# Kernel tuning notes

Measured on AMD Instinct MI355X. Metric: run time of the kernel, lower is better.

Reference implementation:

```python
import jax, jax.numpy as jnp
import numpy as np

NH = 1024
VS = 50257
CUT0 = 1675          # round(VS/30)
CUT1 = 3 * CUT0      # 5025
N_CLUSTERS = 2
HEAD_SIZE = CUT0 + N_CLUSTERS          # 1677
D0, D1 = NH // 4, NH // 16             # 256, 64
SZ0, SZ1 = CUT1 - CUT0, VS - CUT1      # 3350, 45232


def setup_inputs() -> dict:
    key = jax.random.key(0)
    ks = jax.random.split(key, 8)
    s = 0.02
    return {
        "x": jax.random.normal(ks[0], (8, 512, NH), dtype=jnp.float32),
        "y": jax.random.randint(ks[1], (8, 512), 0, VS, dtype=jnp.int64),
        "head_w": jax.random.normal(ks[2], (HEAD_SIZE, NH), dtype=jnp.float32) * s,
        "head_b": jnp.zeros((HEAD_SIZE,), dtype=jnp.float32),
        "proj0": jax.random.normal(ks[3], (D0, NH), dtype=jnp.float32) * s,
        "w0": jax.random.normal(ks[4], (SZ0, D0), dtype=jnp.float32) * s,
        "proj1": jax.random.normal(ks[5], (D1, NH), dtype=jnp.float32) * s,
        "w1": jax.random.normal(ks[6], (SZ1, D1), dtype=jnp.float32) * s,
    }


def reference(x, y, head_w, head_b, proj0, w0, proj1, w1):
    # Flatten as in the torch forward: x -> [N, nh], y -> [N]
    xf = x.reshape(-1, x.shape[-1])            # [N, NH]
    yf = y.reshape(-1)                         # [N]

    # Head: shortlist tokens + 2 cluster logits
    head_logits = jnp.einsum('nh,vh->nv', xf, head_w) + head_b   # [N, 1677]
    head_lp = jax.nn.log_softmax(head_logits, axis=-1)

    # Default: target in head shortlist
    in_head = yf < CUT0
    idx_head = jnp.where(in_head, yf, 0)
    out = jnp.take_along_axis(head_lp, idx_head[:, None], axis=1)[:, 0]

    # Tail clusters: dense per-cluster small GEMMs + log-softmax, masked select
    for i, (low, high, proj, w) in enumerate(
            [(CUT0, CUT1, proj0, w0), (CUT1, VS, proj1, w1)]):
        size = high - low
        h = jnp.einsum('nh,dh->nd', xf, proj)          # [N, d_i]
        lp = jax.nn.log_softmax(jnp.einsum('nd,vd->nv', h, w), axis=-1)  # [N, size]
        rel = jnp.clip(yf - low, 0, size - 1)
        cl = head_lp[:, CUT0 + i] + jnp.take_along_axis(lp, rel[:, None], axis=1)[:, 0]
        mask = (yf >= low) & (yf < high)
        out = jnp.where(mask, cl, out)

    loss = -jnp.mean(out)
    return out, loss
```

## Files before the change

kernel.cpp:

```cpp
#include <hip/hip_runtime.h>
#include <stdint.h>

#define NROWS 4096
#define NHID 1024
#define CC0 1675
#define CC1 5025
#define HEADSZ 1677
#define PD0 256
#define PD1 64
#define TSZ0 3350
#define TSZ1 45232
#define HPN (HEADSZ + PD0 + PD1)
#define TPC1 6
#define L2E 1.4426950408889634f
#define LN2 0.6931471805599453f

#define NB_HD 896
#define NB_PJ 192
#define NB_CW 512
#define NB_MID (NB_HD + NB_PJ + NB_CW)

#define NB_C1 1888
#define NB_C0 864
#define NB_TG 1024
#define NB_TAIL (NB_C1 + NB_C0 + NB_TG)

typedef __attribute__((ext_vector_type(8))) __bf16 bf16x8;
typedef __attribute__((ext_vector_type(4))) float f32x4;

__device__ __forceinline__ unsigned short f2bf(float f) {
  union { float f; uint32_t u; } v; v.f = f;
  return (unsigned short)((v.u + 0x7FFFu + ((v.u >> 16) & 1u)) >> 16);
}
__device__ __forceinline__ float bfl(uint32_t u) {
  union { uint32_t u; float f; } v; v.u = u << 16; return v.f;
}
__device__ __forceinline__ float bfh(uint32_t u) {
  union { uint32_t u; float f; } v; v.u = u & 0xFFFF0000u; return v.f;
}
__device__ __forceinline__ float bf1(unsigned short u) {
  union { uint32_t u; float f; } v; v.u = ((uint32_t)u) << 16; return v.f;
}
#define EXP2(x) __builtin_amdgcn_exp2f(x)

#define CV1 1048576
#define CV2 1477888
#define CV3 1543424
#define CV4 1559808
#define CV5 1774208
#define CV6 2497920
#define CVW0 (CV5 - CV4)
#define CVW  (CV6 - CV4)

__global__ void conv_part(const float* __restrict__ x, const float* __restrict__ hw,
                          const float* __restrict__ p0, const float* __restrict__ p1,
                          unsigned short* __restrict__ dst,
                          const int* __restrict__ y,
                          int* __restrict__ idx0, int* __restrict__ pos0,
                          int* __restrict__ idx1, int* __restrict__ pos1,
                          int* __restrict__ n01,
                          float* __restrict__ hs3, float* __restrict__ outp) {
  if (blockIdx.x >= 1025) {
    int z = blockIdx.x - 1025;
    for (int i = z * 256 + (int)threadIdx.x; i < 3 * NROWS; i += 7 * 256)
      hs3[i] = 0.f;
    if (z == 0 && threadIdx.x == 0) outp[NROWS] = 0.f;
    return;
  }
  if (blockIdx.x == 1024) {
    __shared__ int sc0[256], sc1[256], nsh[2];
    int t = threadIdx.x;
    int yl[16];
    int c0 = 0, c1 = 0;
#pragma unroll
    for (int k = 0; k < 16; ++k) {
      int yv = y[t * 16 + k];
      yl[k] = yv;
      c0 += (yv >= CC0 && yv < CC1);
      c1 += (yv >= CC1);
    }
    sc0[t] = c0; sc1[t] = c1;
    __syncthreads();
    if (t == 0) {
      int a0 = 0, a1 = 0;
      for (int i = 0; i < 256; ++i) {
        int v0 = sc0[i]; sc0[i] = a0; a0 += v0;
        int v1 = sc1[i]; sc1[i] = a1; a1 += v1;
      }
      n01[0] = a0; n01[1] = a1; nsh[0] = a0; nsh[1] = a1;
    }
    __syncthreads();
    int p0c = sc0[t], p1c = sc1[t];
#pragma unroll
    for (int k = 0; k < 16; ++k) {
      int n = t * 16 + k, yv = yl[k];
      if (yv >= CC0 && yv < CC1) { idx0[p0c] = n; pos0[n] = p0c; ++p0c; }
      else if (yv >= CC1)        { idx1[p1c] = n; pos1[n] = p1c; ++p1c; }
    }
    for (int j = nsh[0] + t; j < NROWS; j += 256) idx0[j] = 0;
    for (int j = nsh[1] + t; j < NROWS; j += 256) idx1[j] = 0;
    return;
  }
  const int stride = 1024 * 256;
  for (int i = blockIdx.x * 256 + threadIdx.x; i < CV4; i += stride) {
    const float* src; int off; float sc;
    if (i < CV1)      { src = x;  off = i;       sc = 1.f; }
    else if (i < CV2) { src = hw; off = i - CV1; sc = L2E; }
    else if (i < CV3) { src = p0; off = i - CV2; sc = 1.f; }
    else              { src = p1; off = i - CV3; sc = 1.f; }
    float4 v = reinterpret_cast<const float4*>(src)[off];
    ushort4 o;
    o.x = f2bf(v.x * sc); o.y = f2bf(v.y * sc);
    o.z = f2bf(v.z * sc); o.w = f2bf(v.w * sc);
    reinterpret_cast<ushort4*>(dst)[i] = o;
  }
}

#define GLOAD(g, l) __builtin_amdgcn_global_load_lds( \
    (const __attribute__((address_space(1))) uint32_t*)(const void*)(g), \
    (__attribute__((address_space(3))) uint32_t*)(void*)(l), 16, 0, 0)

#define SWZB(L) ((L) ^ ((((L) >> 7) & 7) << 4))

__device__ __forceinline__
void gemm_core(const unsigned short* __restrict__ A, int lda,
               const unsigned short* __restrict__ B, int ldb,
               int N, int K, int tile0, int tile1, int brow,
               const float* __restrict__ bias,
               float* __restrict__ sum_out,
               unsigned short* __restrict__ Cout, int ldc, int coutStart,
               unsigned short* AsB, unsigned short* BsB,
               const int* __restrict__ gidx) {
  const int tid = threadIdx.x;
  const int lane = tid & 63;
  const int wid = tid >> 6;
  const int wrow = (wid >> 1) * 64;
  const int wcol = (wid & 1) * 64;
  const int lr = lane & 15, lg = lane >> 4;
  const int nsteps = (tile1 - tile0) * (K >> 5);
  const int rowBase = brow + wrow;

  int arowc[2];
#pragma unroll
  for (int c = 0; c < 2; ++c) {
    int g = wid * 128 + c * 64 + lane;
    int S = SWZB(g * 16);
    int row = S >> 6;
    arowc[c] = gidx ? gidx[brow + row] : brow + row;
  }

  float sacc[4][4];
#pragma unroll
  for (int m = 0; m < 4; ++m)
#pragma unroll
    for (int r = 0; r < 4; ++r) sacc[m][r] = 0.f;

  auto stage = [&](int b, int tt, int kk) {
#pragma unroll
    for (int c = 0; c < 2; ++c) {
      int g = wid * 128 + c * 64 + lane;
      int L = g * 16;
      int S = SWZB(L);
      int row = S >> 6, ko = (S >> 4) & 3;
      GLOAD(A + (size_t)arowc[c] * lda + kk + ko * 8, (char*)AsB + b * 8192 + L);
      int bsrc = tt * 128 + row; bsrc = bsrc < N ? bsrc : N - 1;
      GLOAD(B + (size_t)bsrc * ldb + kk + ko * 8, (char*)BsB + b * 8192 + L);
    }
  };

  f32x4 acc[4][4];
#pragma unroll
  for (int m = 0; m < 4; ++m)
#pragma unroll
    for (int n = 0; n < 4; ++n) acc[m][n] = (f32x4){0.f, 0.f, 0.f, 0.f};

  int tp = tile0, kp = 0;
  auto adv = [&](int& t, int& k) { k += 32; if (k == K) { k = 0; ++t; } };
  stage(0, tp, kp); adv(tp, kp);
  if (nsteps > 1) { stage(1, tp, kp); adv(tp, kp); }

  int tile = tile0, k0 = 0;
  for (int s = 0; s < nsteps; ++s) {
    if (s + 1 < nsteps) asm volatile("s_waitcnt vmcnt(4)" ::: "memory");
    else                asm volatile("s_waitcnt vmcnt(0)" ::: "memory");
    __builtin_amdgcn_s_barrier();
    if (s + 2 < nsteps) { stage((s + 2) % 3, tp, kp); adv(tp, kp); }

    const int cur = s % 3;
    int k0n = k0 + 32, tn = tile;
    if (k0n == K) { k0n = 0; tn = tile + 1; }

    bf16x8 af[4], bfv[4];
#pragma unroll
    for (int m = 0; m < 4; ++m)
      af[m] = *(const bf16x8*)((const char*)AsB + cur * 8192 +
                               SWZB((wrow + m * 16 + lr) * 64 + lg * 16));
#pragma unroll
    for (int n = 0; n < 4; ++n)
      bfv[n] = *(const bf16x8*)((const char*)BsB + cur * 8192 +
                                SWZB((wcol + n * 16 + lr) * 64 + lg * 16));
#pragma unroll
    for (int m = 0; m < 4; ++m)
#pragma unroll
      for (int n = 0; n < 4; ++n)
        acc[m][n] = __builtin_amdgcn_mfma_f32_16x16x32_bf16(af[m], bfv[n], acc[m][n], 0, 0, 0);

    if (tn != tile) {
      const int cb = tile * 128 + wcol;
#pragma unroll
      for (int m = 0; m < 4; ++m)
#pragma unroll
        for (int n = 0; n < 4; ++n) {
#pragma unroll
          for (int r = 0; r < 4; ++r) {
            int col = cb + n * 16 + lr;
            if (col < N) {
              float v = acc[m][n][r];
              if (Cout && col >= coutStart) {
                int row = rowBase + m * 16 + lg * 4 + r;
                Cout[(size_t)row * ldc + (col - coutStart)] = f2bf(v);
              } else {
                if (bias) v = fmaf(bias[col], L2E, v);
                sacc[m][r] += EXP2(v);
              }
            }
          }
          acc[m][n] = (f32x4){0.f, 0.f, 0.f, 0.f};
        }
    }
    tile = tn; k0 = k0n;
  }

#pragma unroll
  for (int m = 0; m < 4; ++m)
#pragma unroll
    for (int r = 0; r < 4; ++r) {
      float s = sacc[m][r];
      s += __shfl_xor(s, 1); s += __shfl_xor(s, 2);
      s += __shfl_xor(s, 4); s += __shfl_xor(s, 8);
      if (lr == 0) atomicAdd(&sum_out[rowBase + m * 16 + lg * 4 + r], s);
    }
}

__device__ __forceinline__
void gemm_core4(const unsigned short* __restrict__ A, int lda,
                const unsigned short* __restrict__ B, int ldb,
                int N, int K, int tile0, int brow,
                const float* __restrict__ bias,
                float* __restrict__ sum_out,
                unsigned short* __restrict__ Cout, int ldc,
                char* AsB, char* BsB) {
  const int tid = threadIdx.x;
  const int lane = tid & 63;
  const int wid = tid >> 6;
  const int wrow = (wid >> 1) * 32;
  const int wcol = (wid & 1) * 64;
  const int lr = lane & 15, lg = lane >> 4;
  const int nsteps = K >> 5;
  const int rowBase = brow + wrow;

  const int aL = tid * 16;
  const int aS = SWZB(aL);
  const int arow = aS >> 6, ako = ((aS >> 4) & 3) * 8;
  int bcol[2], bko[2];
#pragma unroll
  for (int c = 0; c < 2; ++c) {
    int L = (c * 256 + tid) * 16;
    int S = SWZB(L);
    int col = S >> 6;
    int bsrc = tile0 * 128 + col;
    bcol[c] = bsrc < N ? bsrc : N - 1;
    bko[c] = ((S >> 4) & 3) * 8;
  }

  auto stage = [&](int b, int kk) {
    GLOAD(A + (size_t)(brow + arow) * lda + kk + ako, AsB + b * 4096 + aL);
#pragma unroll
    for (int c = 0; c < 2; ++c)
      GLOAD(B + (size_t)bcol[c] * ldb + kk + bko[c],
            BsB + b * 8192 + (c * 256 + tid) * 16);
  };

  f32x4 acc[2][4];
#pragma unroll
  for (int m = 0; m < 2; ++m)
#pragma unroll
    for (int n = 0; n < 4; ++n) acc[m][n] = (f32x4){0.f, 0.f, 0.f, 0.f};

  stage(0, 0);
  stage(1, 32);

  for (int s = 0; s < nsteps; ++s) {
    if (s + 1 < nsteps) asm volatile("s_waitcnt vmcnt(3)" ::: "memory");
    else                asm volatile("s_waitcnt vmcnt(0)" ::: "memory");
    __builtin_amdgcn_s_barrier();
    if (s + 2 < nsteps) stage((s + 2) % 3, (s + 2) * 32);

    const int cur = s % 3;
    bf16x8 af[2], bfv[4];
#pragma unroll
    for (int m = 0; m < 2; ++m)
      af[m] = *(const bf16x8*)(AsB + cur * 4096 +
                               SWZB((wrow + m * 16 + lr) * 64 + lg * 16));
#pragma unroll
    for (int n = 0; n < 4; ++n)
      bfv[n] = *(const bf16x8*)(BsB + cur * 8192 +
                                SWZB((wcol + n * 16 + lr) * 64 + lg * 16));
#pragma unroll
    for (int m = 0; m < 2; ++m)
#pragma unroll
      for (int n = 0; n < 4; ++n)
        acc[m][n] = __builtin_amdgcn_mfma_f32_16x16x32_bf16(af[m], bfv[n], acc[m][n], 0, 0, 0);
  }

  const int cb = tile0 * 128 + wcol;
  float sacc[2][4];
#pragma unroll
  for (int m = 0; m < 2; ++m)
#pragma unroll
    for (int r = 0; r < 4; ++r) sacc[m][r] = 0.f;
#pragma unroll
  for (int m = 0; m < 2; ++m)
#pragma unroll
    for (int n = 0; n < 4; ++n)
#pragma unroll
      for (int r = 0; r < 4; ++r) {
        int col = cb + n * 16 + lr;
        if (col < N) {
          float v = acc[m][n][r];
          if (Cout) {
            int row = rowBase + m * 16 + lg * 4 + r;
            Cout[(size_t)row * ldc + col] = f2bf(v);
          } else {
            if (bias) v = fmaf(bias[col], L2E, v);
            sacc[m][r] += EXP2(v);
          }
        }
      }
  if (sum_out) {
#pragma unroll
    for (int m = 0; m < 2; ++m)
#pragma unroll
      for (int r = 0; r < 4; ++r) {
        float s = sacc[m][r];
        s += __shfl_xor(s, 1); s += __shfl_xor(s, 2);
        s += __shfl_xor(s, 4); s += __shfl_xor(s, 8);
        if (lr == 0) atomicAdd(&sum_out[rowBase + m * 16 + lg * 4 + r], s);
      }
  }
}

__global__ __launch_bounds__(256, 4)
void fused_mid(const unsigned short* __restrict__ xb,
               const unsigned short* __restrict__ hpb,
               const float* __restrict__ head_b,
               float* __restrict__ hs,
               unsigned short* __restrict__ hb,
               const float* __restrict__ w0f, const float* __restrict__ w1f,
               unsigned short* __restrict__ dstAll) {
  __shared__ __align__(16) char lds[36864];
  const int bid = blockIdx.x;

  if (bid < NB_HD) {
    const int xcd = bid & 7;
    const int local = bid >> 3;
    const int rowBlk = xcd * 8 + local / 14;
    const int colChunk = local % 14;
    gemm_core4(xb, NHID, hpb, NHID, HEADSZ, NHID, colChunk, rowBlk * 64,
               head_b, hs, nullptr, 0, lds, lds + 12288);
    return;
  }

  if (bid < NB_HD + NB_PJ) {
    const int b1 = bid - NB_HD;
    const int cpx = NB_PJ >> 3;
    const int sid = (b1 & 7) * cpx + (b1 >> 3);
    const int rowBlk = sid & 63;
    const int colChunk = sid >> 6;
    gemm_core4(xb, NHID, hpb + (size_t)HEADSZ * NHID, NHID, PD0 + PD1, NHID,
               colChunk, rowBlk * 64,
               nullptr, nullptr, hb, PD0 + PD1, lds, lds + 12288);
    return;
  }

  {
    const int b2 = bid - NB_HD - NB_PJ;
    const int stride = NB_CW * 256;
    for (int i = b2 * 256 + (int)threadIdx.x; i < CVW; i += stride) {
      const float* src; int off;
      if (i < CVW0) { src = w0f; off = i; }
      else          { src = w1f; off = i - CVW0; }
      float4 v = reinterpret_cast<const float4*>(src)[off];
      ushort4 o;
      o.x = f2bf(v.x * L2E); o.y = f2bf(v.y * L2E);
      o.z = f2bf(v.z * L2E); o.w = f2bf(v.w * L2E);
      reinterpret_cast<ushort4*>(dstAll)[CV4 + i] = o;
    }
  }
}

__global__ __launch_bounds__(256, 3)
void fused_tail(const unsigned short* __restrict__ hb,
                const unsigned short* __restrict__ w0b,
                const unsigned short* __restrict__ w1b,
                const unsigned short* __restrict__ xb,
                const unsigned short* __restrict__ hwb,
                const float* __restrict__ head_b,
                const int* __restrict__ y,
                const int* __restrict__ idx0, const int* __restrict__ idx1,
                const int* __restrict__ n01,
                float* __restrict__ s0, float* __restrict__ s1,
                float* __restrict__ ht, float* __restrict__ tc) {
  __shared__ __align__(16) unsigned short lds[6 * 4096];
  const int bid = blockIdx.x;

  if (bid < NB_C1) {
    const int tid = threadIdx.x;
    const int lane = tid & 63;
    const int wid = tid >> 6;
    const int lr = lane & 15, lg = lane >> 4;
    const int cpx = NB_C1 >> 3;
    const int sid = (bid & 7) * cpx + (bid >> 3);
    const int rowBlk = sid & 31;
    const int colChunk = sid >> 5;
    if (rowBlk * 128 >= n01[1]) return;
    const int rowBase = rowBlk * 128 + (wid >> 1) * 64;
    const int wcol = (wid & 1) * 64;
    const int tile0 = colChunk * TPC1;

    int colOff[4], srcOff[4];
#pragma unroll
    for (int c = 0; c < 4; ++c) {
      int L = (c * 256 + tid) * 16;
      int S = L ^ (((L >> 7) & 7) << 4);
      colOff[c] = S >> 7;
      srcOff[c] = (S & 127) >> 1;
    }
    auto stage = [&](int b, int t) {
#pragma unroll
      for (int c = 0; c < 4; ++c) {
        int gc = t * 128 + colOff[c];
        gc = gc < TSZ1 ? gc : TSZ1 - 1;
        GLOAD(w1b + (size_t)gc * PD1 + srcOff[c],
              (char*)lds + b * 16384 + (c * 256 + tid) * 16);
      }
    };

    bf16x8 af[4][2];
#pragma unroll
    for (int m = 0; m < 4; ++m) {
      int ridx = idx1[rowBase + m * 16 + lr];
      const unsigned short* p = hb + PD0 +
          (size_t)ridx * (PD0 + PD1) + lg * 8;
      af[m][0] = *(const bf16x8*)p;
      af[m][1] = *(const bf16x8*)(p + 32);
    }

    float sacc[4][4];
#pragma unroll
    for (int m = 0; m < 4; ++m)
#pragma unroll
      for (int r = 0; r < 4; ++r) sacc[m][r] = 0.f;

    stage(0, tile0);
    stage(1, tile0 + 1);

#pragma unroll 1
    for (int s = 0; s < TPC1; ++s) {
      if (s + 1 < TPC1) asm volatile("s_waitcnt vmcnt(4)" ::: "memory");
      else              asm volatile("s_waitcnt vmcnt(0)" ::: "memory");
      __builtin_amdgcn_s_barrier();
      if (s + 2 < TPC1) stage((s + 2) % 3, tile0 + s + 2);

      const int cur = s % 3;
      const int cb = (tile0 + s) * 128 + wcol;
      const int full = (cb + 63 < TSZ1);

#pragma unroll
      for (int nh = 0; nh < 2; ++nh) {
        bf16x8 bf[2][2];
#pragma unroll
        for (int nn = 0; nn < 2; ++nn) {
          int ccol = wcol + (nh * 2 + nn) * 16 + lr;
#pragma unroll
          for (int kh = 0; kh < 2; ++kh) {
            int L = ccol * 128 + kh * 64 + lg * 16;
            bf[nn][kh] = *(const bf16x8*)((const char*)lds + cur * 16384 +
                                          (L ^ ((ccol & 7) << 4)));
          }
        }
        f32x4 acc[4][2];
#pragma unroll
        for (int m = 0; m < 4; ++m)
#pragma unroll
          for (int nn = 0; nn < 2; ++nn) {
            f32x4 a = (f32x4){0.f, 0.f, 0.f, 0.f};
            a = __builtin_amdgcn_mfma_f32_16x16x32_bf16(af[m][0], bf[nn][0], a, 0, 0, 0);
            a = __builtin_amdgcn_mfma_f32_16x16x32_bf16(af[m][1], bf[nn][1], a, 0, 0, 0);
            acc[m][nn] = a;
          }
        if (full) {
#pragma unroll
          for (int m = 0; m < 4; ++m)
#pragma unroll
            for (int r = 0; r < 4; ++r)
              sacc[m][r] += EXP2(acc[m][0][r]) + EXP2(acc[m][1][r]);
        } else {
#pragma unroll
          for (int m = 0; m < 4; ++m)
#pragma unroll
            for (int r = 0; r < 4; ++r) {
              float t = 0.f;
#pragma unroll
              for (int nn = 0; nn < 2; ++nn)
                if (cb + (nh * 2 + nn) * 16 + lr < TSZ1) t += EXP2(acc[m][nn][r]);
              sacc[m][r] += t;
            }
        }
      }
    }

#pragma unroll
    for (int m = 0; m < 4; ++m)
#pragma unroll
      for (int r = 0; r < 4; ++r) {
        float s = sacc[m][r];
        s += __shfl_xor(s, 1); s += __shfl_xor(s, 2);
        s += __shfl_xor(s, 4); s += __shfl_xor(s, 8);
        if (lr == 0) atomicAdd(&s1[rowBase + m * 16 + lg * 4 + r], s);
      }
    return;
  }

  if (bid < NB_C1 + NB_C0) {
    const int b0 = bid - NB_C1;
    const int cpx = NB_C0 >> 3;
    const int sid = (b0 & 7) * cpx + (b0 >> 3);
    const int rowBlk = sid & 31;
    const int colChunk = sid >> 5;
    if (rowBlk * 128 >= n01[0]) return;
    gemm_core(hb, PD0 + PD1, w0b, PD0, TSZ0, PD0, colChunk, colChunk + 1,
              rowBlk * 128, nullptr, s0, nullptr, 0, 0,
              (unsigned short*)lds, (unsigned short*)lds + 3 * 4096, idx0);
    return;
  }

  {
    const int b2 = bid - NB_C1 - NB_C0;
    int row = b2 * 4 + (threadIdx.x >> 6);
    int lane = threadIdx.x & 63;
    int yv = y[row];
    int th = yv < CC0 ? yv : (yv < CC1 ? CC0 : CC0 + 1);

    const unsigned short* xr = xb + (size_t)row * NHID + lane * 16;
    const unsigned short* wr = hwb + (size_t)th * NHID + lane * 16;
    uint4 xa = *(const uint4*)xr,       wa = *(const uint4*)wr;
    uint4 xc = *(const uint4*)(xr + 8), wc = *(const uint4*)(wr + 8);
    float s = 0.f;
    uint32_t xs[8] = {xa.x, xa.y, xa.z, xa.w, xc.x, xc.y, xc.z, xc.w};
    uint32_t ws[8] = {wa.x, wa.y, wa.z, wa.w, wc.x, wc.y, wc.z, wc.w};
#pragma unroll
    for (int j = 0; j < 8; ++j)
      s += bfl(xs[j]) * bfl(ws[j]) + bfh(xs[j]) * bfh(ws[j]);
#pragma unroll
    for (int d = 1; d < 64; d <<= 1) s += __shfl_xor(s, d);

    float cl = 0.f;
    if (yv >= CC0) {
      if (yv < CC1) {
        int rel = yv - CC0;
        const unsigned short* hr = hb + (size_t)row * (PD0 + PD1) + lane * 4;
        const unsigned short* w0r = w0b + (size_t)rel * PD0 + lane * 4;
        uint2 ha = *(const uint2*)hr, wa0 = *(const uint2*)w0r;
        cl = bfl(ha.x) * bfl(wa0.x) + bfh(ha.x) * bfh(wa0.x)
           + bfl(ha.y) * bfl(wa0.y) + bfh(ha.y) * bfh(wa0.y);
      } else {
        int rel = yv - CC1;
        cl = bf1(hb[(size_t)row * (PD0 + PD1) + PD0 + lane])
           * bf1(w1b[(size_t)rel * PD1 + lane]);
      }
#pragma unroll
      for (int d = 1; d < 64; d <<= 1) cl += __shfl_xor(cl, d);
    }
    if (lane == 0) { ht[row] = s * LN2 + head_b[th]; tc[row] = (yv < CC0) ? 0.f : cl; }
  }
}

__global__ void rowloss(const float* __restrict__ hs, const float* __restrict__ ht,
                        const float* __restrict__ s0, const float* __restrict__ s1,
                        const float* __restrict__ tc,
                        const int* __restrict__ pos0, const int* __restrict__ pos1,
                        const int* __restrict__ y, float* __restrict__ out) {
  int n = blockIdx.x * 256 + threadIdx.x;
  int yv = y[n];
  float o = ht[n] - __builtin_amdgcn_logf(hs[n]) * LN2;
  if (yv >= CC0) {
    float sv = (yv < CC1) ? s0[pos0[n]] : s1[pos1[n]];
    o += tc[n] * LN2 - __builtin_amdgcn_logf(sv) * LN2;
  }
  out[n] = o;
  float l = o;
#pragma unroll
  for (int d = 1; d < 64; d <<= 1) l += __shfl_xor(l, d);
  __shared__ float red[4];
  if ((threadIdx.x & 63) == 0) red[threadIdx.x >> 6] = l;
  __syncthreads();
  if (threadIdx.x == 0)
    atomicAdd(&out[NROWS], -(red[0] + red[1] + red[2] + red[3]) / (float)NROWS);
}

extern "C" void kernel_launch(void* const* d_in, const int* in_sizes, int n_in,
                              void* d_out, int out_size, void* d_ws, size_t ws_size,
                              hipStream_t stream) {
  const float* x      = (const float*)d_in[0];
  const int*   y      = (const int*)d_in[1];
  const float* head_w = (const float*)d_in[2];
  const float* head_b = (const float*)d_in[3];
  const float* proj0  = (const float*)d_in[4];
  const float* w0     = (const float*)d_in[5];
  const float* proj1  = (const float*)d_in[6];
  const float* w1     = (const float*)d_in[7];
  float* out = (float*)d_out;

  char* wp = (char*)d_ws;
  unsigned short* xb  = (unsigned short*)wp; wp += (size_t)NROWS * NHID * 2;
  unsigned short* hpb = (unsigned short*)wp; wp += (size_t)HPN * NHID * 2;
  unsigned short* w0b = (unsigned short*)wp; wp += (size_t)TSZ0 * PD0 * 2;
  unsigned short* w1b = (unsigned short*)wp; wp += (size_t)TSZ1 * PD1 * 2;
  unsigned short* hb  = (unsigned short*)wp; wp += (size_t)NROWS * (PD0 + PD1) * 2;
  float* hs = (float*)wp; wp += NROWS * 4;
  float* s0 = (float*)wp; wp += NROWS * 4;
  float* s1 = (float*)wp; wp += NROWS * 4;
  float* ht = (float*)wp; wp += NROWS * 4;
  float* tc = (float*)wp; wp += NROWS * 4;
  int* idx0 = (int*)wp; wp += NROWS * 4;
  int* pos0 = (int*)wp; wp += NROWS * 4;
  int* idx1 = (int*)wp; wp += NROWS * 4;
  int* pos1 = (int*)wp; wp += NROWS * 4;
  int* n01  = (int*)wp; wp += 8 * 4;

  conv_part<<<dim3(1032), 256, 0, stream>>>(
      x, head_w, proj0, proj1, xb, y, idx0, pos0, idx1, pos1, n01, hs, out);

  fused_mid<<<dim3(NB_MID), 256, 0, stream>>>(
      xb, hpb, head_b, hs, hb, w0, w1, xb);

  fused_tail<<<dim3(NB_TAIL), 256, 0, stream>>>(
      hb, w0b, w1b, xb, hpb, head_b, y, idx0, idx1, n01, s0, s1, ht, tc);

  rowloss<<<dim3(NROWS / 256), 256, 0, stream>>>(
      hs, ht, s0, s1, tc, pos0, pos1, y, out);
}
```

Measured before the change: 96.70 us.

## Move head GEMM into tail kernel and tail weight conversion into first pass

The head-logit GEMM blocks move from the middle kernel into the tail kernel, so they can run concurrently with the cluster GEMMs. The middle kernel shrinks to just the small projection GEMM. Conversion of the cluster weight matrices to bf16 moves into the initial conversion kernel. The goal is to shorten the critical path and cut idle time between dependent launches, at the cost of a longer first conversion pass and more contention for resources inside the tail kernel.

```diff
diff --git a/kernel.cpp b/kernel.cpp
--- a/kernel.cpp
+++ b/kernel.cpp
@@ -15,15 +15,13 @@
 #define L2E 1.4426950408889634f
 #define LN2 0.6931471805599453f
 
+#define NB_PJ 192
+
 #define NB_HD 896
-#define NB_PJ 192
-#define NB_CW 512
-#define NB_MID (NB_HD + NB_PJ + NB_CW)
-
 #define NB_C1 1888
 #define NB_C0 864
 #define NB_TG 1024
-#define NB_TAIL (NB_C1 + NB_C0 + NB_TG)
+#define NB_TAIL (NB_HD + NB_C1 + NB_C0 + NB_TG)
 
 typedef __attribute__((ext_vector_type(8))) __bf16 bf16x8;
 typedef __attribute__((ext_vector_type(4))) float f32x4;
@@ -49,11 +47,10 @@
 #define CV4 1559808
 #define CV5 1774208
 #define CV6 2497920
-#define CVW0 (CV5 - CV4)
-#define CVW  (CV6 - CV4)
 
 __global__ void conv_part(const float* __restrict__ x, const float* __restrict__ hw,
                           const float* __restrict__ p0, const float* __restrict__ p1,
+                          const float* __restrict__ w0, const float* __restrict__ w1,
                           unsigned short* __restrict__ dst,
                           const int* __restrict__ y,
                           int* __restrict__ idx0, int* __restrict__ pos0,
@@ -102,12 +99,14 @@
     return;
   }
   const int stride = 1024 * 256;
-  for (int i = blockIdx.x * 256 + threadIdx.x; i < CV4; i += stride) {
+  for (int i = blockIdx.x * 256 + threadIdx.x; i < CV6; i += stride) {
     const float* src; int off; float sc;
     if (i < CV1)      { src = x;  off = i;       sc = 1.f; }
     else if (i < CV2) { src = hw; off = i - CV1; sc = L2E; }
     else if (i < CV3) { src = p0; off = i - CV2; sc = 1.f; }
-    else              { src = p1; off = i - CV3; sc = 1.f; }
+    else if (i < CV4) { src = p1; off = i - CV3; sc = 1.f; }
+    else if (i < CV5) { src = w0; off = i - CV4; sc = L2E; }
+    else              { src = w1; off = i - CV5; sc = L2E; }
     float4 v = reinterpret_cast<const float4*>(src)[off];
     ushort4 o;
     o.x = f2bf(v.x * sc); o.y = f2bf(v.y * sc);
@@ -351,52 +350,18 @@
 }
 
 __global__ __launch_bounds__(256, 4)
-void fused_mid(const unsigned short* __restrict__ xb,
-               const unsigned short* __restrict__ hpb,
-               const float* __restrict__ head_b,
-               float* __restrict__ hs,
-               unsigned short* __restrict__ hb,
-               const float* __restrict__ w0f, const float* __restrict__ w1f,
-               unsigned short* __restrict__ dstAll) {
+void proj_mid(const unsigned short* __restrict__ xb,
+              const unsigned short* __restrict__ hpb,
+              unsigned short* __restrict__ hb) {
   __shared__ __align__(16) char lds[36864];
   const int bid = blockIdx.x;
-
-  if (bid < NB_HD) {
-    const int xcd = bid & 7;
-    const int local = bid >> 3;
-    const int rowBlk = xcd * 8 + local / 14;
-    const int colChunk = local % 14;
-    gemm_core4(xb, NHID, hpb, NHID, HEADSZ, NHID, colChunk, rowBlk * 64,
-               head_b, hs, nullptr, 0, lds, lds + 12288);
-    return;
-  }
-
-  if (bid < NB_HD + NB_PJ) {
-    const int b1 = bid - NB_HD;
-    const int cpx = NB_PJ >> 3;
-    const int sid = (b1 & 7) * cpx + (b1 >> 3);
-    const int rowBlk = sid & 63;
-    const int colChunk = sid >> 6;
-    gemm_core4(xb, NHID, hpb + (size_t)HEADSZ * NHID, NHID, PD0 + PD1, NHID,
-               colChunk, rowBlk * 64,
-               nullptr, nullptr, hb, PD0 + PD1, lds, lds + 12288);
-    return;
-  }
-
-  {
-    const int b2 = bid - NB_HD - NB_PJ;
-    const int stride = NB_CW * 256;
-    for (int i = b2 * 256 + (int)threadIdx.x; i < CVW; i += stride) {
-      const float* src; int off;
-      if (i < CVW0) { src = w0f; off = i; }
-      else          { src = w1f; off = i - CVW0; }
-      float4 v = reinterpret_cast<const float4*>(src)[off];
-      ushort4 o;
-      o.x = f2bf(v.x * L2E); o.y = f2bf(v.y * L2E);
-      o.z = f2bf(v.z * L2E); o.w = f2bf(v.w * L2E);
-      reinterpret_cast<ushort4*>(dstAll)[CV4 + i] = o;
-    }
-  }
+  const int cpx = NB_PJ >> 3;
+  const int sid = (bid & 7) * cpx + (bid >> 3);
+  const int rowBlk = sid & 63;
+  const int colChunk = sid >> 6;
+  gemm_core4(xb, NHID, hpb + (size_t)HEADSZ * NHID, NHID, PD0 + PD1, NHID,
+             colChunk, rowBlk * 64,
+             nullptr, nullptr, hb, PD0 + PD1, lds, lds + 12288);
 }
 
 __global__ __launch_bounds__(256, 3)
@@ -409,18 +374,30 @@
                 const int* __restrict__ y,
                 const int* __restrict__ idx0, const int* __restrict__ idx1,
                 const int* __restrict__ n01,
+                float* __restrict__ hs,
                 float* __restrict__ s0, float* __restrict__ s1,
                 float* __restrict__ ht, float* __restrict__ tc) {
   __shared__ __align__(16) unsigned short lds[6 * 4096];
   const int bid = blockIdx.x;
 
-  if (bid < NB_C1) {
+  if (bid < NB_HD) {
+    const int xcd = bid & 7;
+    const int local = bid >> 3;
+    const int rowBlk = xcd * 8 + local / 14;
+    const int colChunk = local % 14;
+    gemm_core4(xb, NHID, hwb, NHID, HEADSZ, NHID, colChunk, rowBlk * 64,
+               head_b, hs, nullptr, 0, (char*)lds, (char*)lds + 12288);
+    return;
+  }
+
+  if (bid < NB_HD + NB_C1) {
+    const int b1 = bid - NB_HD;
     const int tid = threadIdx.x;
     const int lane = tid & 63;
     const int wid = tid >> 6;
     const int lr = lane & 15, lg = lane >> 4;
     const int cpx = NB_C1 >> 3;
-    const int sid = (bid & 7) * cpx + (bid >> 3);
+    const int sid = (b1 & 7) * cpx + (b1 >> 3);
     const int rowBlk = sid & 31;
     const int colChunk = sid >> 5;
     if (rowBlk * 128 >= n01[1]) return;
@@ -532,8 +509,8 @@
     return;
   }
 
-  if (bid < NB_C1 + NB_C0) {
-    const int b0 = bid - NB_C1;
+  if (bid < NB_HD + NB_C1 + NB_C0) {
+    const int b0 = bid - NB_HD - NB_C1;
     const int cpx = NB_C0 >> 3;
     const int sid = (b0 & 7) * cpx + (b0 >> 3);
     const int rowBlk = sid & 31;
@@ -546,7 +523,7 @@
   }
 
   {
-    const int b2 = bid - NB_C1 - NB_C0;
+    const int b2 = bid - NB_HD - NB_C1 - NB_C0;
     int row = b2 * 4 + (threadIdx.x >> 6);
     int lane = threadIdx.x & 63;
     int yv = y[row];
@@ -640,13 +617,13 @@
   int* n01  = (int*)wp; wp += 8 * 4;
 
   conv_part<<<dim3(1032), 256, 0, stream>>>(
-      x, head_w, proj0, proj1, xb, y, idx0, pos0, idx1, pos1, n01, hs, out);
-
-  fused_mid<<<dim3(NB_MID), 256, 0, stream>>>(
-      xb, hpb, head_b, hs, hb, w0, w1, xb);
+      x, head_w, proj0, proj1, w0, w1, xb, y,
+      idx0, pos0, idx1, pos1, n01, hs, out);
+
+  proj_mid<<<dim3(NB_PJ), 256, 0, stream>>>(xb, hpb, hb);
 
   fused_tail<<<dim3(NB_TAIL), 256, 0, stream>>>(
-      hb, w0b, w1b, xb, hpb, head_b, y, idx0, idx1, n01, s0, s1, ht, tc);
+      hb, w0b, w1b, xb, hpb, head_b, y, idx0, idx1, n01, hs, s0, s1, ht, tc);
 
   rowloss<<<dim3(NROWS / 256), 256, 0, stream>>>(
       hs, ht, s0, s1, tc, pos0, pos1, y, out);
```

New measurement: 93.13 us, median of 2. 1.04x faster.
